# Performance work log

Measured on AMD Instinct MI355X. Metric: run time of the kernel, lower is better.

The kernel has to match this reference:

```python
import jax, jax.numpy as jnp
import numpy as np

CUTOFF = 6.0   # matches init cutoff
D = 32         # descriptor/MLP width
NTYPES = 3     # len(type_map)


def setup_inputs() -> dict:
    key = jax.random.key(0)
    ks = jax.random.split(key, 13)
    b, n, m, n_ghost = 2, 8192, 64, 512
    neighbor_vectors = jax.random.normal(ks[0], (b, n, m, 4), jnp.float32)
    element_map = jax.random.randint(ks[1], (b, n), 0, NTYPES, jnp.int32)
    central_atoms = jax.random.randint(ks[2], (b, n), 0, n, jnp.int32)
    neighbor_indices = jax.random.randint(ks[3], (b, n, m), 0, n + n_ghost, jnp.int32)
    neighbor_types = jax.random.randint(ks[4], (b, n, m), 0, NTYPES, jnp.int32)
    type_embed = 0.1 * jax.random.normal(ks[5], (NTYPES, D), jnp.float32)
    elem_bias = 0.1 * jax.random.normal(ks[6], (NTYPES,), jnp.float32)
    W1 = 0.5 * jax.random.normal(ks[7], (4, D), jnp.float32)
    b1 = 0.1 * jax.random.normal(ks[8], (D,), jnp.float32)
    W2 = (1.0 / np.sqrt(D)) * jax.random.normal(ks[9], (D, D), jnp.float32)
    b2 = 0.1 * jax.random.normal(ks[10], (D,), jnp.float32)
    W3 = (1.0 / np.sqrt(D)) * jax.random.normal(ks[11], (D, 1), jnp.float32)
    b3 = 0.1 * jax.random.normal(ks[12], (1,), jnp.float32)
    return dict(element_map=element_map, central_atoms=central_atoms,
                neighbor_indices=neighbor_indices, neighbor_types=neighbor_types,
                neighbor_vectors=neighbor_vectors, n_ghost=n_ghost,
                type_embed=type_embed, elem_bias=elem_bias,
                W1=W1, b1=b1, W2=W2, b2=b2, W3=W3, b3=b3)


def _field_Ei(rel, element_map, neighbor_types, type_embed, elem_bias, W1, b1, W2, b2, W3, b3):
    # rel: [b,n,m,3] relative positions; recompute distance as the torch forward does
    dist = jnp.linalg.norm(rel, axis=-1, keepdims=True)                 # [b,n,m,1]
    fc = 0.5 * (jnp.cos(jnp.pi * jnp.minimum(dist, CUTOFF) / CUTOFF) + 1.0)
    s = jnp.exp(-dist) * fc                                             # smooth radial weight
    feat = jnp.concatenate([s, s * rel], axis=-1)                       # [b,n,m,4]
    h = jnp.tanh(feat @ W1 + b1 + type_embed[neighbor_types])           # [b,n,m,D]
    g = h.mean(axis=2)                                                  # pool over neighbors -> [b,n,D]
    h2 = jnp.tanh(g @ W2 + b2)                                          # [b,n,D]
    Ei = h2 @ W3 + b3 + elem_bias[element_map][..., None]               # [b,n,1]
    return Ei


def derive_mechanics(grad_Ei, neighbor_vectors, neighbor_indices, n_ghost):
    # grad_Ei: [b,n,m,3] = d(sum Ei)/d r_ij, with r_ij = r_j - r_i
    b, n, m, _ = grad_Ei.shape
    ntot = n + n_ghost
    bidx = jnp.arange(b)[:, None, None]
    # force on central atom i: +sum_j dE/dr_ij ; reaction scattered to neighbor j: -dE/dr_ij
    force = jnp.zeros((b, ntot, 3), grad_Ei.dtype)
    force = force.at[:, :n].add(grad_Ei.sum(axis=2))
    force = force.at[bidx, neighbor_indices].add(-grad_Ei)
    rij = neighbor_vectors[..., 1:]                                     # [b,n,m,3]
    pv = (rij[..., :, None] * grad_Ei[..., None, :]).reshape(b, n, m, 9)  # pair virial r (x) dE
    virial = pv.sum(axis=(1, 2))                                        # [b,9]
    av = jnp.zeros((b, ntot, 9), grad_Ei.dtype)
    av = av.at[bidx, neighbor_indices].add(pv)
    return force[:, :n], virial, av[:, :n]


def reference(element_map, central_atoms, neighbor_indices, neighbor_types,
              neighbor_vectors, n_ghost, type_embed, elem_bias,
              W1, b1, W2, b2, W3, b3):
    rel = neighbor_vectors[..., 1:]                                     # [b,n,m,3]

    def ei_sum(r):
        Ei = _field_Ei(r, element_map, neighbor_types, type_embed, elem_bias,
                       W1, b1, W2, b2, W3, b3)
        return Ei.sum(), Ei

    grad_Ei, Ei = jax.grad(ei_sum, has_aux=True)(rel)                   # matches autograd.grad w/ ones mask
    Etot = Ei.sum(axis=1)                                               # [b,1]
    dist = jnp.linalg.norm(rel, axis=-1, keepdims=True)
    nv = jnp.concatenate([dist, rel], axis=-1)
    force, virial, atomic_virial = derive_mechanics(grad_Ei, nv, neighbor_indices, n_ghost)
    return Etot, Ei, force, virial, atomic_virial
```

## Files before the change

kernel.cpp:

```cpp
#include <hip/hip_runtime.h>

#define CUTOFF_F 6.0f
#define PI_F 3.14159265358979323846f
#define CAP 112
#define EXCAP 8192

typedef __fp16 fp16x2 __attribute__((ext_vector_type(2)));

__device__ __forceinline__ unsigned pk2(float a, float b) {
  union { fp16x2 h; unsigned u; } cv;
  cv.h = __builtin_amdgcn_cvt_pkrtz(a, b);
  return cv.u;
}
__device__ __forceinline__ float f16bits(unsigned v) {
  union { unsigned short u; __fp16 h; } cv; cv.u = (unsigned short)v; return (float)cv.h;
}

template<int CTRL>
__device__ __forceinline__ float dpp_add(float x) {
  int y = __builtin_amdgcn_update_dpp(0, __float_as_int(x), CTRL, 0xf, 0xf, true);
  return x + __int_as_float(y);
}
__device__ __forceinline__ float wave_sum63(float x) {
  x = dpp_add<0x111>(x);
  x = dpp_add<0x112>(x);
  x = dpp_add<0x114>(x);
  x = dpp_add<0x118>(x);
  x = dpp_add<0x142>(x);
  x = dpp_add<0x143>(x);
  return x;
}

__device__ __forceinline__ float fast_tanh(float x) {
  float e = __expf(2.0f * x);
  return 1.0f - 2.0f * __builtin_amdgcn_rcpf(e + 1.0f);
}

__global__ __launch_bounds__(256) void field_zero(
    int* __restrict__ counts, int* __restrict__ ecount, int bn) {
  const int i = blockIdx.x * 256 + threadIdx.x;
  if (i < bn) counts[i] = 0;
  if (i == 0) ecount[0] = 0;
}

__global__ __launch_bounds__(256) void field_main(
    const int* __restrict__ element_map,
    const int* __restrict__ neighbor_indices,
    const int* __restrict__ neighbor_types,
    const float4* __restrict__ neighbor_vectors,
    const float* __restrict__ type_embed,
    const float* __restrict__ elem_bias,
    const float* __restrict__ W1,
    const float* __restrict__ b1,
    const float* __restrict__ W2,
    const float* __restrict__ b2,
    const float* __restrict__ W3,
    const float* __restrict__ b3,
    float* __restrict__ outEi,
    int* __restrict__ counts,
    int* __restrict__ ecount,
    float4* __restrict__ extras,
    float4* __restrict__ bucket,
    float* __restrict__ partials,
    int n)
{
  __shared__ float4 sW1t[32];
  __shared__ float  sbte[3][32];
  __shared__ float  sW2[32 * 33];
  __shared__ float  sW3[32];
  __shared__ float  sb2[32];
  __shared__ float  sElemBias[3];
  __shared__ float  sb3;
  __shared__ float  blkEi[4];
  __shared__ float  blkVir[4][9];
  __shared__ unsigned hb[4][64][9];
  __shared__ float    gtd[4][3][32];

  const int tid = threadIdx.x;

  if (tid < 32) {
    sW1t[tid] = make_float4(W1[tid], W1[32 + tid], W1[64 + tid], W1[96 + tid]);
    sW3[tid]  = W3[tid];
    sb2[tid]  = b2[tid];
  } else if (tid < 128) {
    int t = (tid - 32) >> 5, k = tid & 31;
    sbte[t][k] = b1[k] + type_embed[t * 32 + k];
  } else if (tid == 128) {
    sb3 = b3[0];
  } else if (tid < 132) {
    sElemBias[tid - 129] = elem_bias[tid - 129];
  }
  for (int i = tid; i < 1024; i += 256) {
    int l = i >> 5, k = i & 31;
    sW2[l * 33 + k] = W2[i];
  }
  __syncthreads();

  const int wave = tid >> 6;
  const int lane = tid & 63;
  const int atom = blockIdx.x * 4 + wave;
  const int bb = atom / n;

  const int base = atom * 64 + lane;
  const int idx = neighbor_indices[base];
  const int dest = bb * n + idx;
  const int em = element_map[atom];

  int pos = 0;
  const bool real = (idx < n);
  if (real) pos = atomicAdd(&counts[dest], 1);

  const float4 nv = neighbor_vectors[base];
  const float rx = nv.y, ry = nv.z, rz = nv.w;
  const int typ = neighbor_types[base];

  const float d2 = rx * rx + ry * ry + rz * rz;
  const float d = sqrtf(d2);
  const float invd = (d > 0.0f) ? __builtin_amdgcn_rcpf(d) : 0.0f;
  float s, sp;
  if (d < CUTOFF_F) {
    const float arg = d * (PI_F / CUTOFF_F);
    const float cs = __cosf(arg);
    const float sn = __sinf(arg);
    const float e = __expf(-d);
    const float fc = 0.5f * (cs + 1.0f);
    const float fcp = -(0.5f * PI_F / CUTOFF_F) * sn;
    s = e * fc;
    sp = e * (fcp - fc);
  } else {
    s = 0.0f;
    sp = 0.0f;
  }
  const float f1 = s * rx, f2 = s * ry, f3 = s * rz;

  float h[32];
  const int dim = lane & 15;
  const int q   = lane >> 4;
  const int w   = dim >> 1;
  const int sh  = (dim & 1) << 4;

#pragma unroll
  for (int pass = 0; pass < 2; ++pass) {
    const int kb = pass << 4;
#pragma unroll
    for (int k = 0; k < 16; k += 2) {
      const float4 wa = sW1t[kb + k];
      float pa = sbte[typ][kb + k];
      pa = fmaf(s, wa.x, pa); pa = fmaf(f1, wa.y, pa);
      pa = fmaf(f2, wa.z, pa); pa = fmaf(f3, wa.w, pa);
      h[kb + k] = fast_tanh(pa);
      const float4 wb = sW1t[kb + k + 1];
      float pb = sbte[typ][kb + k + 1];
      pb = fmaf(s, wb.x, pb); pb = fmaf(f1, wb.y, pb);
      pb = fmaf(f2, wb.z, pb); pb = fmaf(f3, wb.w, pb);
      h[kb + k + 1] = fast_tanh(pb);
      hb[wave][lane][k >> 1] = pk2(h[kb + k], h[kb + k + 1]);
    }
    float s0 = 0.0f, s1 = 0.0f;
#pragma unroll
    for (int jj = 0; jj < 16; jj += 2) {
      s0 += f16bits(hb[wave][(q << 4) + jj][w] >> sh);
      s1 += f16bits(hb[wave][(q << 4) + jj + 1][w] >> sh);
    }
    float gs = s0 + s1;
    gs += __shfl_xor(gs, 16);
    gs += __shfl_xor(gs, 32);
    if (lane < 16) gtd[wave][0][kb + lane] = gs * (1.0f / 64.0f);
  }

  const int kd = lane & 31;
  float a0 = sb2[kd], a1 = 0.0f, a2 = 0.0f, a3 = 0.0f;
#pragma unroll
  for (int l = 0; l < 8; l += 4) {
    const float4 gA = *(const float4*)&gtd[wave][0][l];
    const float4 gB = *(const float4*)&gtd[wave][0][l + 8];
    const float4 gC = *(const float4*)&gtd[wave][0][l + 16];
    const float4 gD = *(const float4*)&gtd[wave][0][l + 24];
    a0 = fmaf(gA.x, sW2[(l + 0) * 33 + kd], a0);
    a0 = fmaf(gA.y, sW2[(l + 1) * 33 + kd], a0);
    a0 = fmaf(gA.z, sW2[(l + 2) * 33 + kd], a0);
    a0 = fmaf(gA.w, sW2[(l + 3) * 33 + kd], a0);
    a1 = fmaf(gB.x, sW2[(l + 8) * 33 + kd], a1);
    a1 = fmaf(gB.y, sW2[(l + 9) * 33 + kd], a1);
    a1 = fmaf(gB.z, sW2[(l + 10) * 33 + kd], a1);
    a1 = fmaf(gB.w, sW2[(l + 11) * 33 + kd], a1);
    a2 = fmaf(gC.x, sW2[(l + 16) * 33 + kd], a2);
    a2 = fmaf(gC.y, sW2[(l + 17) * 33 + kd], a2);
    a2 = fmaf(gC.z, sW2[(l + 18) * 33 + kd], a2);
    a2 = fmaf(gC.w, sW2[(l + 19) * 33 + kd], a2);
    a3 = fmaf(gD.x, sW2[(l + 24) * 33 + kd], a3);
    a3 = fmaf(gD.y, sW2[(l + 25) * 33 + kd], a3);
    a3 = fmaf(gD.z, sW2[(l + 26) * 33 + kd], a3);
    a3 = fmaf(gD.w, sW2[(l + 27) * 33 + kd], a3);
  }
  const float acc = (a0 + a1) + (a2 + a3);
  const float h2 = fast_tanh(acc);
  const float tl = (1.0f - h2 * h2) * sW3[kd];
  if (lane < 32) gtd[wave][1][kd] = tl;

  float b0 = 0.0f, b1v = 0.0f, b2v = 0.0f, b3v = 0.0f;
#pragma unroll
  for (int l = 0; l < 8; l += 4) {
    const float4 tA = *(const float4*)&gtd[wave][1][l];
    const float4 tB = *(const float4*)&gtd[wave][1][l + 8];
    const float4 tC = *(const float4*)&gtd[wave][1][l + 16];
    const float4 tD = *(const float4*)&gtd[wave][1][l + 24];
    b0 = fmaf(tA.x, sW2[kd * 33 + l + 0], b0);
    b0 = fmaf(tA.y, sW2[kd * 33 + l + 1], b0);
    b0 = fmaf(tA.z, sW2[kd * 33 + l + 2], b0);
    b0 = fmaf(tA.w, sW2[kd * 33 + l + 3], b0);
    b1v = fmaf(tB.x, sW2[kd * 33 + l + 8], b1v);
    b1v = fmaf(tB.y, sW2[kd * 33 + l + 9], b1v);
    b1v = fmaf(tB.z, sW2[kd * 33 + l + 10], b1v);
    b1v = fmaf(tB.w, sW2[kd * 33 + l + 11], b1v);
    b2v = fmaf(tC.x, sW2[kd * 33 + l + 16], b2v);
    b2v = fmaf(tC.y, sW2[kd * 33 + l + 17], b2v);
    b2v = fmaf(tC.z, sW2[kd * 33 + l + 18], b2v);
    b2v = fmaf(tC.w, sW2[kd * 33 + l + 19], b2v);
    b3v = fmaf(tD.x, sW2[kd * 33 + l + 24], b3v);
    b3v = fmaf(tD.y, sW2[kd * 33 + l + 25], b3v);
    b3v = fmaf(tD.z, sW2[kd * 33 + l + 26], b3v);
    b3v = fmaf(tD.w, sW2[kd * 33 + l + 27], b3v);
  }
  if (lane < 32) gtd[wave][2][kd] = ((b0 + b1v) + (b2v + b3v)) * (1.0f / 64.0f);

  float p = h2 * sW3[kd];

  float q0 = 0.0f, q1 = 0.0f, q2 = 0.0f, q3 = 0.0f;
#pragma unroll
  for (int k = 0; k < 32; k += 4) {
    const float4 d4 = *(const float4*)&gtd[wave][2][k];
#pragma unroll
    for (int u = 0; u < 4; ++u) {
      const float dgk = (u == 0) ? d4.x : (u == 1) ? d4.y : (u == 2) ? d4.z : d4.w;
      const float hk = h[k + u];
      const float dpre = dgk * (1.0f - hk * hk);
      const float4 wv = sW1t[k + u];
      q0 = fmaf(dpre, wv.x, q0);
      q1 = fmaf(dpre, wv.y, q1);
      q2 = fmaf(dpre, wv.z, q2);
      q3 = fmaf(dpre, wv.w, q3);
    }
  }

  const float common = sp * invd * (q0 + q1 * rx + q2 * ry + q3 * rz);
  const float gx = fmaf(common, rx, s * q1);
  const float gy = fmaf(common, ry, s * q2);
  const float gz = fmaf(common, rz, s * q3);

  if (real) {
    float4 pay;
    pay.x = __uint_as_float(pk2(gx, gy));
    pay.y = __uint_as_float(pk2(gz, rx));
    pay.z = __uint_as_float(pk2(ry, rz));
    if (pos < CAP) {
      pay.w = 0.0f;
      bucket[(size_t)dest * CAP + pos] = pay;
    } else {
      const int ep = atomicAdd(ecount, 1);
      if (ep < EXCAP) {
        pay.w = __int_as_float(dest);
        extras[ep] = pay;
      }
    }
  }

  float sfx = wave_sum63(gx);
  float sfy = wave_sum63(gy);
  float sfz = wave_sum63(gz);
  float vr0 = wave_sum63(rx * gx), vr1 = wave_sum63(rx * gy), vr2 = wave_sum63(rx * gz);
  float vr3 = wave_sum63(ry * gx), vr4 = wave_sum63(ry * gy), vr5 = wave_sum63(ry * gz);
  float vr6 = wave_sum63(rz * gx), vr7 = wave_sum63(rz * gy), vr8 = wave_sum63(rz * gz);
  float psum = wave_sum63(p) * 0.5f;

  if (lane == 63) {
    const float Ei_val = psum + sb3 + sElemBias[em];
    outEi[atom] = Ei_val;
    blkEi[wave] = Ei_val;
    blkVir[wave][0] = vr0; blkVir[wave][1] = vr1; blkVir[wave][2] = vr2;
    blkVir[wave][3] = vr3; blkVir[wave][4] = vr4; blkVir[wave][5] = vr5;
    blkVir[wave][6] = vr6; blkVir[wave][7] = vr7; blkVir[wave][8] = vr8;
    float4 pay;
    pay.x = __uint_as_float(pk2(-sfx, -sfy));
    pay.y = __uint_as_float(pk2(-sfz, 0.0f));
    pay.z = 0.0f;
    const int spos = atomicAdd(&counts[atom], 1);
    if (spos < CAP) {
      pay.w = 0.0f;
      bucket[(size_t)atom * CAP + spos] = pay;
    } else {
      const int ep = atomicAdd(ecount, 1);
      if (ep < EXCAP) {
        pay.w = __int_as_float(atom);
        extras[ep] = pay;
      }
    }
  }

  __syncthreads();
  if (tid < 9) {
    partials[blockIdx.x * 10 + tid] =
        blkVir[0][tid] + blkVir[1][tid] + blkVir[2][tid] + blkVir[3][tid];
  } else if (tid == 9) {
    partials[blockIdx.x * 10 + 9] = blkEi[0] + blkEi[1] + blkEi[2] + blkEi[3];
  }
}

__global__ __launch_bounds__(256) void field_gather(
    const int* __restrict__ counts,
    const int* __restrict__ ecount,
    const float4* __restrict__ extras,
    const float4* __restrict__ bucket,
    const float* __restrict__ partials,
    float* __restrict__ outForce,
    float* __restrict__ outAV,
    float* __restrict__ outEtot,
    float* __restrict__ outVirial,
    int half)
{
  __shared__ float sf[4][12];
  __shared__ float sacc[4][10];
  const int tid = threadIdx.x;
  const int wave = tid >> 6;
  const int lane = tid & 63;
  const int dest = blockIdx.x * 4 + wave;

  const int rawcnt = counts[dest];
  const int cnt = (rawcnt > CAP) ? CAP : rawcnt;
  const int ec0 = *ecount;

  float fx = 0.0f, fy = 0.0f, fz = 0.0f;
  float a0 = 0, a1 = 0, a2 = 0, a3 = 0, a4 = 0, a5 = 0, a6 = 0, a7 = 0, a8 = 0;

#pragma unroll 2
  for (int l = lane; l < cnt; l += 64) {
    const float4 pay = bucket[(size_t)dest * CAP + l];
    const unsigned w0 = __float_as_uint(pay.x);
    const unsigned w1 = __float_as_uint(pay.y);
    const unsigned w2 = __float_as_uint(pay.z);
    const float gx = f16bits(w0), gy = f16bits(w0 >> 16);
    const float gz = f16bits(w1), rx = f16bits(w1 >> 16);
    const float ry = f16bits(w2), rz = f16bits(w2 >> 16);
    fx -= gx; fy -= gy; fz -= gz;
    a0 = fmaf(rx, gx, a0); a1 = fmaf(rx, gy, a1); a2 = fmaf(rx, gz, a2);
    a3 = fmaf(ry, gx, a3); a4 = fmaf(ry, gy, a4); a5 = fmaf(ry, gz, a5);
    a6 = fmaf(rz, gx, a6); a7 = fmaf(rz, gy, a7); a8 = fmaf(rz, gz, a8);
  }

  if (ec0 > 0) {
    const int ec = (ec0 < EXCAP) ? ec0 : EXCAP;
    for (int t = lane; t < ec; t += 64) {
      const float4 ex = extras[t];
      if (__float_as_int(ex.w) == dest) {
        const unsigned w0 = __float_as_uint(ex.x);
        const unsigned w1 = __float_as_uint(ex.y);
        const unsigned w2 = __float_as_uint(ex.z);
        const float gx = f16bits(w0), gy = f16bits(w0 >> 16);
        const float gz = f16bits(w1), rx = f16bits(w1 >> 16);
        const float ry = f16bits(w2), rz = f16bits(w2 >> 16);
        fx -= gx; fy -= gy; fz -= gz;
        a0 = fmaf(rx, gx, a0); a1 = fmaf(rx, gy, a1); a2 = fmaf(rx, gz, a2);
        a3 = fmaf(ry, gx, a3); a4 = fmaf(ry, gy, a4); a5 = fmaf(ry, gz, a5);
        a6 = fmaf(rz, gx, a6); a7 = fmaf(rz, gy, a7); a8 = fmaf(rz, gz, a8);
      }
    }
  }

  fx = wave_sum63(fx); fy = wave_sum63(fy); fz = wave_sum63(fz);
  a0 = wave_sum63(a0); a1 = wave_sum63(a1); a2 = wave_sum63(a2);
  a3 = wave_sum63(a3); a4 = wave_sum63(a4); a5 = wave_sum63(a5);
  a6 = wave_sum63(a6); a7 = wave_sum63(a7); a8 = wave_sum63(a8);

  if (lane == 63) {
    sf[wave][0] = fx; sf[wave][1] = fy; sf[wave][2] = fz;
    sf[wave][3] = a0; sf[wave][4] = a1; sf[wave][5] = a2;
    sf[wave][6] = a3; sf[wave][7] = a4; sf[wave][8] = a5;
    sf[wave][9] = a6; sf[wave][10] = a7; sf[wave][11] = a8;
  }
  __syncthreads();

  const int d0 = blockIdx.x * 4;
  if (tid < 12) {
    outForce[(size_t)d0 * 3 + tid] = sf[tid / 3][tid % 3];
  } else if (tid >= 64 && tid < 100) {
    const int t = tid - 64;
    outAV[(size_t)d0 * 9 + t] = sf[t / 9][3 + t % 9];
  }

  if (blockIdx.x < 2) {
    const int b = blockIdx.x;
    float acc[10] = {0, 0, 0, 0, 0, 0, 0, 0, 0, 0};
    for (int r = b * half + tid; r < (b + 1) * half; r += 256) {
#pragma unroll
      for (int t = 0; t < 10; ++t) acc[t] += partials[r * 10 + t];
    }
#pragma unroll
    for (int t = 0; t < 10; ++t) acc[t] = wave_sum63(acc[t]);
    if (lane == 63) {
#pragma unroll
      for (int t = 0; t < 10; ++t) sacc[wave][t] = acc[t];
    }
    __syncthreads();
    if (tid < 9) {
      outVirial[b * 9 + tid] = sacc[0][tid] + sacc[1][tid] + sacc[2][tid] + sacc[3][tid];
    } else if (tid == 9) {
      outEtot[b] = sacc[0][9] + sacc[1][9] + sacc[2][9] + sacc[3][9];
    }
  }
}

extern "C" void kernel_launch(void* const* d_in, const int* in_sizes, int n_in,
                              void* d_out, int out_size, void* d_ws, size_t ws_size,
                              hipStream_t stream) {
  const int* element_map        = (const int*)d_in[0];
  const int* neighbor_indices   = (const int*)d_in[2];
  const int* neighbor_types     = (const int*)d_in[3];
  const float4* neighbor_vectors = (const float4*)d_in[4];
  const float* type_embed = (const float*)d_in[6];
  const float* elem_bias  = (const float*)d_in[7];
  const float* W1 = (const float*)d_in[8];
  const float* b1 = (const float*)d_in[9];
  const float* W2 = (const float*)d_in[10];
  const float* b2 = (const float*)d_in[11];
  const float* W3 = (const float*)d_in[12];
  const float* b3 = (const float*)d_in[13];

  const int B = 2;
  const int bn = in_sizes[0];
  const int n = bn / B;
  const int nblk = bn / 4;

  float* out = (float*)d_out;
  float* outEtot   = out;
  float* outEi     = outEtot + B;
  float* outForce  = outEi + bn;
  float* outVirial = outForce + (size_t)bn * 3;
  float* outAV     = outVirial + (size_t)B * 9;

  char* ws = (char*)d_ws;
  int* counts = (int*)ws;
  size_t countBytes = (size_t)bn * sizeof(int);
  int* ecount = (int*)(ws + countBytes);
  size_t ecountBytes = 16;
  float4* extras = (float4*)(ws + countBytes + ecountBytes);
  size_t extrasBytes = (size_t)EXCAP * sizeof(float4);
  float* partials = (float*)(ws + countBytes + ecountBytes + extrasBytes);
  size_t partialBytes = (size_t)nblk * 10 * sizeof(float);
  float4* bucket = (float4*)(ws + countBytes + ecountBytes + extrasBytes + partialBytes);

  dim3 block(256);
  hipLaunchKernelGGL(field_zero, dim3((bn + 255) / 256), block, 0, stream,
                     counts, ecount, bn);
  hipLaunchKernelGGL(field_main, dim3(nblk), block, 0, stream,
                     element_map, neighbor_indices, neighbor_types,
                     neighbor_vectors, type_embed, elem_bias,
                     W1, b1, W2, b2, W3, b3,
                     outEi, counts, ecount, extras, bucket, partials, n);
  hipLaunchKernelGGL(field_gather, dim3(nblk), block, 0, stream,
                     counts, ecount, extras, bucket, partials,
                     outForce, outAV, outEtot, outVirial, nblk / B);
}
```

Before: 147.2 us.

## Split W2 matvecs across wave halves and gather with 16 lanes per atom

In the main kernel, the two 32x32 W2 matrix-vector products (forward and backward) are split so each half of the wave covers 16 of the 32 input rows. The two halves are then combined with a single cross-half shuffle, which halves the per-lane FMA and LDS-read work. The gather kernel now gives each destination atom 16 lanes instead of a full 64-lane wave, packing 16 atoms per block, and reduces with a row-level DPP sum. This cuts idle lanes and the number of gather blocks. The cost is longer per-lane loops over the bucket, and a slower scan of the overflow extras list when it is non-empty.

Measured after the change: 146.4 us. Within noise of the previous version (-0.5%).

```diff
diff --git a/kernel.cpp b/kernel.cpp
--- a/kernel.cpp
+++ b/kernel.cpp
@@ -28,6 +28,13 @@
   x = dpp_add<0x118>(x);
   x = dpp_add<0x142>(x);
   x = dpp_add<0x143>(x);
+  return x;
+}
+__device__ __forceinline__ float row_sum15(float x) {
+  x = dpp_add<0x111>(x);
+  x = dpp_add<0x112>(x);
+  x = dpp_add<0x114>(x);
+  x = dpp_add<0x118>(x);
   return x;
 }
 
@@ -65,7 +72,7 @@
     int n)
 {
   __shared__ float4 sW1t[32];
-  __shared__ float  sbte[3][32];
+  __shared__ float  sbte[3][33];
   __shared__ float  sW2[32 * 33];
   __shared__ float  sW3[32];
   __shared__ float  sb2[32];
@@ -169,60 +176,63 @@
   }
 
   const int kd = lane & 31;
-  float a0 = sb2[kd], a1 = 0.0f, a2 = 0.0f, a3 = 0.0f;
-#pragma unroll
-  for (int l = 0; l < 8; l += 4) {
-    const float4 gA = *(const float4*)&gtd[wave][0][l];
-    const float4 gB = *(const float4*)&gtd[wave][0][l + 8];
-    const float4 gC = *(const float4*)&gtd[wave][0][l + 16];
-    const float4 gD = *(const float4*)&gtd[wave][0][l + 24];
-    a0 = fmaf(gA.x, sW2[(l + 0) * 33 + kd], a0);
-    a0 = fmaf(gA.y, sW2[(l + 1) * 33 + kd], a0);
-    a0 = fmaf(gA.z, sW2[(l + 2) * 33 + kd], a0);
-    a0 = fmaf(gA.w, sW2[(l + 3) * 33 + kd], a0);
-    a1 = fmaf(gB.x, sW2[(l + 8) * 33 + kd], a1);
-    a1 = fmaf(gB.y, sW2[(l + 9) * 33 + kd], a1);
-    a1 = fmaf(gB.z, sW2[(l + 10) * 33 + kd], a1);
-    a1 = fmaf(gB.w, sW2[(l + 11) * 33 + kd], a1);
-    a2 = fmaf(gC.x, sW2[(l + 16) * 33 + kd], a2);
-    a2 = fmaf(gC.y, sW2[(l + 17) * 33 + kd], a2);
-    a2 = fmaf(gC.z, sW2[(l + 18) * 33 + kd], a2);
-    a2 = fmaf(gC.w, sW2[(l + 19) * 33 + kd], a2);
-    a3 = fmaf(gD.x, sW2[(l + 24) * 33 + kd], a3);
-    a3 = fmaf(gD.y, sW2[(l + 25) * 33 + kd], a3);
-    a3 = fmaf(gD.z, sW2[(l + 26) * 33 + kd], a3);
-    a3 = fmaf(gD.w, sW2[(l + 27) * 33 + kd], a3);
-  }
-  const float acc = (a0 + a1) + (a2 + a3);
+  const int lb = (lane >> 5) << 4;
+  float a0 = (lane < 32) ? sb2[kd] : 0.0f;
+  float a1 = 0.0f;
+  {
+    const float4 gA = *(const float4*)&gtd[wave][0][lb];
+    const float4 gB = *(const float4*)&gtd[wave][0][lb + 4];
+    const float4 gC = *(const float4*)&gtd[wave][0][lb + 8];
+    const float4 gD = *(const float4*)&gtd[wave][0][lb + 12];
+    a0 = fmaf(gA.x, sW2[(lb + 0) * 33 + kd], a0);
+    a0 = fmaf(gA.y, sW2[(lb + 1) * 33 + kd], a0);
+    a0 = fmaf(gA.z, sW2[(lb + 2) * 33 + kd], a0);
+    a0 = fmaf(gA.w, sW2[(lb + 3) * 33 + kd], a0);
+    a1 = fmaf(gB.x, sW2[(lb + 4) * 33 + kd], a1);
+    a1 = fmaf(gB.y, sW2[(lb + 5) * 33 + kd], a1);
+    a1 = fmaf(gB.z, sW2[(lb + 6) * 33 + kd], a1);
+    a1 = fmaf(gB.w, sW2[(lb + 7) * 33 + kd], a1);
+    a0 = fmaf(gC.x, sW2[(lb + 8) * 33 + kd], a0);
+    a0 = fmaf(gC.y, sW2[(lb + 9) * 33 + kd], a0);
+    a0 = fmaf(gC.z, sW2[(lb + 10) * 33 + kd], a0);
+    a0 = fmaf(gC.w, sW2[(lb + 11) * 33 + kd], a0);
+    a1 = fmaf(gD.x, sW2[(lb + 12) * 33 + kd], a1);
+    a1 = fmaf(gD.y, sW2[(lb + 13) * 33 + kd], a1);
+    a1 = fmaf(gD.z, sW2[(lb + 14) * 33 + kd], a1);
+    a1 = fmaf(gD.w, sW2[(lb + 15) * 33 + kd], a1);
+  }
+  float acc = a0 + a1;
+  acc += __shfl_xor(acc, 32);
   const float h2 = fast_tanh(acc);
   const float tl = (1.0f - h2 * h2) * sW3[kd];
   if (lane < 32) gtd[wave][1][kd] = tl;
 
-  float b0 = 0.0f, b1v = 0.0f, b2v = 0.0f, b3v = 0.0f;
-#pragma unroll
-  for (int l = 0; l < 8; l += 4) {
-    const float4 tA = *(const float4*)&gtd[wave][1][l];
-    const float4 tB = *(const float4*)&gtd[wave][1][l + 8];
-    const float4 tC = *(const float4*)&gtd[wave][1][l + 16];
-    const float4 tD = *(const float4*)&gtd[wave][1][l + 24];
-    b0 = fmaf(tA.x, sW2[kd * 33 + l + 0], b0);
-    b0 = fmaf(tA.y, sW2[kd * 33 + l + 1], b0);
-    b0 = fmaf(tA.z, sW2[kd * 33 + l + 2], b0);
-    b0 = fmaf(tA.w, sW2[kd * 33 + l + 3], b0);
-    b1v = fmaf(tB.x, sW2[kd * 33 + l + 8], b1v);
-    b1v = fmaf(tB.y, sW2[kd * 33 + l + 9], b1v);
-    b1v = fmaf(tB.z, sW2[kd * 33 + l + 10], b1v);
-    b1v = fmaf(tB.w, sW2[kd * 33 + l + 11], b1v);
-    b2v = fmaf(tC.x, sW2[kd * 33 + l + 16], b2v);
-    b2v = fmaf(tC.y, sW2[kd * 33 + l + 17], b2v);
-    b2v = fmaf(tC.z, sW2[kd * 33 + l + 18], b2v);
-    b2v = fmaf(tC.w, sW2[kd * 33 + l + 19], b2v);
-    b3v = fmaf(tD.x, sW2[kd * 33 + l + 24], b3v);
-    b3v = fmaf(tD.y, sW2[kd * 33 + l + 25], b3v);
-    b3v = fmaf(tD.z, sW2[kd * 33 + l + 26], b3v);
-    b3v = fmaf(tD.w, sW2[kd * 33 + l + 27], b3v);
-  }
-  if (lane < 32) gtd[wave][2][kd] = ((b0 + b1v) + (b2v + b3v)) * (1.0f / 64.0f);
+  float b0 = 0.0f, b1v = 0.0f;
+  {
+    const float4 tA = *(const float4*)&gtd[wave][1][lb];
+    const float4 tB = *(const float4*)&gtd[wave][1][lb + 4];
+    const float4 tC = *(const float4*)&gtd[wave][1][lb + 8];
+    const float4 tD = *(const float4*)&gtd[wave][1][lb + 12];
+    b0 = fmaf(tA.x, sW2[kd * 33 + lb + 0], b0);
+    b0 = fmaf(tA.y, sW2[kd * 33 + lb + 1], b0);
+    b0 = fmaf(tA.z, sW2[kd * 33 + lb + 2], b0);
+    b0 = fmaf(tA.w, sW2[kd * 33 + lb + 3], b0);
+    b1v = fmaf(tB.x, sW2[kd * 33 + lb + 4], b1v);
+    b1v = fmaf(tB.y, sW2[kd * 33 + lb + 5], b1v);
+    b1v = fmaf(tB.z, sW2[kd * 33 + lb + 6], b1v);
+    b1v = fmaf(tB.w, sW2[kd * 33 + lb + 7], b1v);
+    b0 = fmaf(tC.x, sW2[kd * 33 + lb + 8], b0);
+    b0 = fmaf(tC.y, sW2[kd * 33 + lb + 9], b0);
+    b0 = fmaf(tC.z, sW2[kd * 33 + lb + 10], b0);
+    b0 = fmaf(tC.w, sW2[kd * 33 + lb + 11], b0);
+    b1v = fmaf(tD.x, sW2[kd * 33 + lb + 12], b1v);
+    b1v = fmaf(tD.y, sW2[kd * 33 + lb + 13], b1v);
+    b1v = fmaf(tD.z, sW2[kd * 33 + lb + 14], b1v);
+    b1v = fmaf(tD.w, sW2[kd * 33 + lb + 15], b1v);
+  }
+  float dg = b0 + b1v;
+  dg += __shfl_xor(dg, 32);
+  if (lane < 32) gtd[wave][2][kd] = dg * (1.0f / 64.0f);
 
   float p = h2 * sW3[kd];
 
@@ -318,12 +328,14 @@
     float* __restrict__ outVirial,
     int half)
 {
-  __shared__ float sf[4][12];
+  __shared__ float sf[16][12];
   __shared__ float sacc[4][10];
   const int tid = threadIdx.x;
   const int wave = tid >> 6;
   const int lane = tid & 63;
-  const int dest = blockIdx.x * 4 + wave;
+  const int grp = tid >> 4;
+  const int sub = tid & 15;
+  const int dest = blockIdx.x * 16 + grp;
 
   const int rawcnt = counts[dest];
   const int cnt = (rawcnt > CAP) ? CAP : rawcnt;
@@ -332,9 +344,10 @@
   float fx = 0.0f, fy = 0.0f, fz = 0.0f;
   float a0 = 0, a1 = 0, a2 = 0, a3 = 0, a4 = 0, a5 = 0, a6 = 0, a7 = 0, a8 = 0;
 
+  const float4* row = bucket + (size_t)dest * CAP;
 #pragma unroll 2
-  for (int l = lane; l < cnt; l += 64) {
-    const float4 pay = bucket[(size_t)dest * CAP + l];
+  for (int l = sub; l < cnt; l += 16) {
+    const float4 pay = row[l];
     const unsigned w0 = __float_as_uint(pay.x);
     const unsigned w1 = __float_as_uint(pay.y);
     const unsigned w2 = __float_as_uint(pay.z);
@@ -349,7 +362,7 @@
 
   if (ec0 > 0) {
     const int ec = (ec0 < EXCAP) ? ec0 : EXCAP;
-    for (int t = lane; t < ec; t += 64) {
+    for (int t = sub; t < ec; t += 16) {
       const float4 ex = extras[t];
       if (__float_as_int(ex.w) == dest) {
         const unsigned w0 = __float_as_uint(ex.x);
@@ -366,23 +379,24 @@
     }
   }
 
-  fx = wave_sum63(fx); fy = wave_sum63(fy); fz = wave_sum63(fz);
-  a0 = wave_sum63(a0); a1 = wave_sum63(a1); a2 = wave_sum63(a2);
-  a3 = wave_sum63(a3); a4 = wave_sum63(a4); a5 = wave_sum63(a5);
-  a6 = wave_sum63(a6); a7 = wave_sum63(a7); a8 = wave_sum63(a8);
-
-  if (lane == 63) {
-    sf[wave][0] = fx; sf[wave][1] = fy; sf[wave][2] = fz;
-    sf[wave][3] = a0; sf[wave][4] = a1; sf[wave][5] = a2;
-    sf[wave][6] = a3; sf[wave][7] = a4; sf[wave][8] = a5;
-    sf[wave][9] = a6; sf[wave][10] = a7; sf[wave][11] = a8;
+  fx = row_sum15(fx); fy = row_sum15(fy); fz = row_sum15(fz);
+  a0 = row_sum15(a0); a1 = row_sum15(a1); a2 = row_sum15(a2);
+  a3 = row_sum15(a3); a4 = row_sum15(a4); a5 = row_sum15(a5);
+  a6 = row_sum15(a6); a7 = row_sum15(a7); a8 = row_sum15(a8);
+
+  if (sub == 15) {
+    float* o = sf[grp];
+    o[0] = fx; o[1] = fy; o[2] = fz;
+    o[3] = a0; o[4] = a1; o[5] = a2;
+    o[6] = a3; o[7] = a4; o[8] = a5;
+    o[9] = a6; o[10] = a7; o[11] = a8;
   }
   __syncthreads();
 
-  const int d0 = blockIdx.x * 4;
-  if (tid < 12) {
+  const int d0 = blockIdx.x * 16;
+  if (tid < 48) {
     outForce[(size_t)d0 * 3 + tid] = sf[tid / 3][tid % 3];
-  } else if (tid >= 64 && tid < 100) {
+  } else if (tid >= 64 && tid < 208) {
     const int t = tid - 64;
     outAV[(size_t)d0 * 9 + t] = sf[t / 9][3 + t % 9];
   }
@@ -456,7 +470,7 @@
                      neighbor_vectors, type_embed, elem_bias,
                      W1, b1, W2, b2, W3, b3,
                      outEi, counts, ecount, extras, bucket, partials, n);
-  hipLaunchKernelGGL(field_gather, dim3(nblk), block, 0, stream,
+  hipLaunchKernelGGL(field_gather, dim3(bn / 16), block, 0, stream,
                      counts, ecount, extras, bucket, partials,
                      outForce, outAV, outEtot, outVirial, nblk / B);
 }
```
